# Optimization experiments

Measured on AMD Instinct MI355X. Metric: run time of the kernel, lower is better.

Reference implementation:

```python
import jax, jax.numpy as jnp
import numpy as np

APERTURE = 128
LN_EPS = 1e-6

def _layer_norm(y, g, b):
    mu = jnp.mean(y, axis=-1, keepdims=True)
    var = jnp.var(y, axis=-1, keepdims=True)
    return (y - mu) / jnp.sqrt(var + LN_EPS) * g + b

def setup_inputs() -> dict:
    key = jax.random.key(0)
    ks = jax.random.split(key, 12)
    B, S, D = 4, 4096, 1024
    gain = np.sqrt(2.0)
    xav = lambda k, fan_out, fan_in: jax.random.uniform(
        k, (fan_out, fan_in), jnp.float32,
        -gain * np.sqrt(6.0 / (fan_in + fan_out)), gain * np.sqrt(6.0 / (fan_in + fan_out)))
    return {
        "x": jax.random.normal(ks[0], (B, S, D), jnp.float32),
        "Wq": xav(ks[1], D, D),
        "Wk": xav(ks[2], D, D),
        "Wv": xav(ks[3], D, D),
        "Wo": xav(ks[4], D, D),
        "k1_w": xav(ks[5], D, D),
        "k1_b": jnp.full((D,), 0.1, jnp.float32),
        "k2_w": xav(ks[6], 1, D),
        "k2_b": jnp.full((1,), 0.1, jnp.float32),
        "ln_g": jnp.ones((D,), jnp.float32),
        "ln_b": jnp.zeros((D,), jnp.float32),
    }

def reference(x, Wq, Wk, Wv, Wo, k1_w, k1_b, k2_w, k2_b, ln_g, ln_b):
    B, S, D = x.shape
    scale = jnp.float32(1.0 / np.sqrt(D))
    neg_inf = jnp.float32(-np.inf)

    Q = x @ Wq.T  # [B,S,D]
    K = x @ Wk.T
    V = x @ Wv.T

    e = jnp.einsum('bsd,btd->bst', Q, K) * scale  # [B,S,S]

    # ignore_self: -inf on the diagonal
    i = jnp.arange(S)[:, None]
    j = jnp.arange(S)[None, :]
    e = jnp.where(i == j, neg_inf, e)

    # banded aperture mask: tril(e, ap) * triu(e, -ap); zeros of the product -> -inf
    d = j - i
    scope = jnp.where(d <= APERTURE, e, 0.0) * jnp.where(d >= -APERTURE, e, 0.0)
    e = jnp.where(scope == 0.0, neg_inf, e)

    alpha = jax.nn.softmax(e, axis=2)
    c = jnp.einsum('bst,btd->bsd', alpha, V)
    c = c @ Wo.T

    y = c + x
    y = _layer_norm(y, ln_g, ln_b)
    y = jax.nn.relu(y @ k1_w.T + k1_b)
    y = _layer_norm(y, ln_g, ln_b)
    y = jax.nn.sigmoid(y @ k2_w.T + k2_b)  # [B,S,1]
    return y.reshape(B, S)
```

## Files before the change

kernel.cpp:

```cpp
#include <hip/hip_runtime.h>
#include <math.h>

#define DD 1024
#define SS 4096
#define AP 128
#define LN_EPS 1e-6f
#define BK 32
#define BAND 384

typedef __bf16 bf16;
typedef __attribute__((ext_vector_type(4))) __bf16 bf16x4;
typedef __attribute__((ext_vector_type(8))) __bf16 bf16x8;
typedef __attribute__((ext_vector_type(4))) float f32x4;

#define GLOAD_LDS16(g, l)                                                   \
    __builtin_amdgcn_global_load_lds(                                        \
        (const __attribute__((address_space(1))) void*)(g),                  \
        (__attribute__((address_space(3))) void*)(l), 16, 0, 0)

__global__ __launch_bounds__(256) void prep_all(const float* __restrict__ x,
                                                const float* __restrict__ Wq,
                                                const float* __restrict__ Wk,
                                                const float* __restrict__ Wv,
                                                const float* __restrict__ Wo,
                                                const float* __restrict__ k1w,
                                                const float* __restrict__ k1b,
                                                const float* __restrict__ lng,
                                                const float* __restrict__ lnb,
                                                bf16* __restrict__ xb,
                                                bf16* __restrict__ Wob,
                                                bf16* __restrict__ k1g,
                                                bf16* __restrict__ Wtb,
                                                float* __restrict__ u1,
                                                float* __restrict__ c1b) {
    __shared__ float tile[64][65];
    const int bid = blockIdx.x;
    const int tid = threadIdx.x;
    if (bid < 16384) {
        const int i = (bid * 256 + tid) * 4;
        const float4 a = *(const float4*)(x + i);
        bf16x4 o;
        o[0] = (__bf16)a.x; o[1] = (__bf16)a.y; o[2] = (__bf16)a.z; o[3] = (__bf16)a.w;
        *(bf16x4*)(xb + i) = o;
        return;
    }
    if (bid < 18432) {
        const int b2 = bid - 16384;
        const int sel = b2 >> 10;
        const int bb = b2 & 1023;
        const float* s = sel ? k1w : Wo;
        bf16* d = sel ? k1g : Wob;
        const int i = (bb * 256 + tid) * 4;
        float4 a = *(const float4*)(s + i);
        if (sel) {
            const float4 g4 = *(const float4*)(lng + (i & (DD - 1)));
            a.x *= g4.x; a.y *= g4.y; a.z *= g4.z; a.w *= g4.w;
        }
        bf16x4 o;
        o[0] = (__bf16)a.x; o[1] = (__bf16)a.y; o[2] = (__bf16)a.z; o[3] = (__bf16)a.w;
        *(bf16x4*)(d + i) = o;
        return;
    }
    if (bid < 19200) {
        const int t = bid - 18432;
        const int tz = t >> 8;
        const int tb_ = t & 255;
        const float* in = (tz == 0) ? Wq : (tz == 1) ? Wk : Wv;
        bf16* out = Wtb + ((size_t)tz << 20);
        const int r0 = (tb_ >> 4) * 64, c0 = (tb_ & 15) * 64;
        const int lr = tid >> 4;
        const int lc = (tid & 15) * 4;
#pragma unroll
        for (int rr = 0; rr < 4; rr++) {
            const int row = lr + rr * 16;
            const float4 v = *(const float4*)(in + (size_t)(r0 + row) * DD + c0 + lc);
            tile[row][lc] = v.x; tile[row][lc + 1] = v.y;
            tile[row][lc + 2] = v.z; tile[row][lc + 3] = v.w;
        }
        __syncthreads();
#pragma unroll
        for (int rr = 0; rr < 4; rr++) {
            const int row = lr + rr * 16;
            bf16x4 o;
            o[0] = (__bf16)tile[lc + 0][row];
            o[1] = (__bf16)tile[lc + 1][row];
            o[2] = (__bf16)tile[lc + 2][row];
            o[3] = (__bf16)tile[lc + 3][row];
            *(bf16x4*)(out + (size_t)(c0 + row) * DD + r0 + lc) = o;
        }
        return;
    }
    const int pv = bid - 19200;
    const int lane = tid & 63, wave = tid >> 6;
    const int n = pv * 4 + wave;
    const float* row = k1w + (size_t)n * DD + lane * 16;
    float su = 0.f, sb = 0.f;
#pragma unroll
    for (int q = 0; q < 4; q++) {
        const float4 a = *(const float4*)(row + q * 4);
        const float4 g4 = *(const float4*)(lng + lane * 16 + q * 4);
        const float4 b4 = *(const float4*)(lnb + lane * 16 + q * 4);
        su += a.x * g4.x + a.y * g4.y + a.z * g4.z + a.w * g4.w;
        sb += a.x * b4.x + a.y * b4.y + a.z * b4.z + a.w * b4.w;
    }
#pragma unroll
    for (int off = 32; off > 0; off >>= 1) {
        su += __shfl_xor(su, off);
        sb += __shfl_xor(sb, off);
    }
    if (lane == 0) {
        u1[n] = su;
        c1b[n] = sb + k1b[n];
    }
}

__global__ __launch_bounds__(256) void gemm_pair(const bf16* __restrict__ A0,
                                                 const bf16* __restrict__ W0,
                                                 bf16* __restrict__ O0,
                                                 const bf16* __restrict__ A1,
                                                 const bf16* __restrict__ W1,
                                                 bf16* __restrict__ O1) {
    const bf16* A = blockIdx.z ? A1 : A0;
    const bf16* W = blockIdx.z ? W1 : W0;
    bf16* O = blockIdx.z ? O1 : O0;
    __shared__ bf16 As[128 * BK];
    __shared__ bf16 Bs[128 * BK];
    const int tid = threadIdx.x;
    const int lane = tid & 63;
    const int wave = tid >> 6;
    const int wm = wave & 1;
    const int wn = wave >> 1;
    const int m0 = blockIdx.y * 128;
    const int n0 = blockIdx.x * 128;

    const int c = wave * 64 + lane;
    const int ar = c >> 2;
    const int ac = (c & 3) << 3;
    char* AsB = (char*)As;
    char* BsB = (char*)Bs;
    const int lr = lane & 15;
    const int lk = (lane >> 4) << 3;

    f32x4 acc[4][4] = {};

    for (int kt = 0; kt < DD; kt += BK) {
        const bf16* ga0 = A + (size_t)(m0 + ar) * DD + kt + ac;
        const bf16* gb0 = W + (size_t)(n0 + ar) * DD + kt + ac;
        GLOAD_LDS16(ga0, AsB + wave * 1024);
        GLOAD_LDS16(ga0 + (size_t)64 * DD, AsB + 4096 + wave * 1024);
        GLOAD_LDS16(gb0, BsB + wave * 1024);
        GLOAD_LDS16(gb0 + (size_t)64 * DD, BsB + 4096 + wave * 1024);
        __syncthreads();

        bf16x8 af[4], bfr[4];
#pragma unroll
        for (int i = 0; i < 4; i++)
            af[i] = *(const bf16x8*)&As[(wm * 64 + i * 16 + lr) * BK + lk];
#pragma unroll
        for (int j = 0; j < 4; j++)
            bfr[j] = *(const bf16x8*)&Bs[(wn * 64 + j * 16 + lr) * BK + lk];
#pragma unroll
        for (int i = 0; i < 4; i++)
#pragma unroll
            for (int j = 0; j < 4; j++)
                acc[i][j] = __builtin_amdgcn_mfma_f32_16x16x32_bf16(af[i], bfr[j], acc[i][j], 0, 0, 0);
        __syncthreads();
    }

#pragma unroll
    for (int i = 0; i < 4; i++) {
        const int row = m0 + wm * 64 + i * 16 + ((lane >> 4) << 2);
#pragma unroll
        for (int j = 0; j < 4; j++) {
            const int col = n0 + wn * 64 + j * 16 + (lane & 15);
#pragma unroll
            for (int rr = 0; rr < 4; rr++)
                O[(size_t)(row + rr) * DD + col] = (__bf16)acc[i][j][rr];
        }
    }
}


#define KL_STAGE_A(tt, hh, bb)                                               \
    {                                                                        \
        const bf16* gp_ = Aop + gofsA + (tt) * 64 + (hh) * 32;               \
        GLOAD_LDS16(gp_, smem + (bb) + (hh) * 16384 + ldsW);                 \
        GLOAD_LDS16(gp_ + (size_t)128 * DD,                                  \
                    smem + (bb) + (hh) * 16384 + 8192 + ldsW);               \
    }
#define KL_STAGE_B(tt, hh, bb)                                               \
    {                                                                        \
        const bf16* gp_ = Bop + gofsB + (tt) * 64 + (hh) * 32;               \
        GLOAD_LDS16(gp_, smem + (bb) + 32768 + (hh) * 16384 + ldsW);         \
        GLOAD_LDS16(gp_ + (size_t)128 * DD,                                  \
                    smem + (bb) + 32768 + (hh) * 16384 + 8192 + ldsW);       \
    }
#define KL_READS_A(ks, mh)                                                   \
    af[0] = *(const bf16x8*)(sA + bufo + (ks) * 16384 + (mh) * 4096);        \
    af[1] = *(const bf16x8*)(sA + bufo + (ks) * 16384 + (mh) * 4096 + 1024); \
    af[2] = *(const bf16x8*)(sA + bufo + (ks) * 16384 + (mh) * 4096 + 2048); \
    af[3] = *(const bf16x8*)(sA + bufo + (ks) * 16384 + (mh) * 4096 + 3072);
#define KL_READS_B(ks)                                                       \
    bfr[0] = *(const bf16x8*)(sB + bufo + (ks) * 16384);                     \
    bfr[1] = *(const bf16x8*)(sB + bufo + (ks) * 16384 + 1024);              \
    bfr[2] = *(const bf16x8*)(sB + bufo + (ks) * 16384 + 2048);              \
    bfr[3] = *(const bf16x8*)(sB + bufo + (ks) * 16384 + 3072);
#define KL_MFMA4(I, MH)                                                      \
    acc[(MH) * 4 + I][0] = __builtin_amdgcn_mfma_f32_16x16x32_bf16(af[I], bfr[0], acc[(MH) * 4 + I][0], 0, 0, 0); \
    acc[(MH) * 4 + I][1] = __builtin_amdgcn_mfma_f32_16x16x32_bf16(af[I], bfr[1], acc[(MH) * 4 + I][1], 0, 0, 0); \
    acc[(MH) * 4 + I][2] = __builtin_amdgcn_mfma_f32_16x16x32_bf16(af[I], bfr[2], acc[(MH) * 4 + I][2], 0, 0, 0); \
    acc[(MH) * 4 + I][3] = __builtin_amdgcn_mfma_f32_16x16x32_bf16(af[I], bfr[3], acc[(MH) * 4 + I][3], 0, 0, 0);
#define KL_MFMA16(MH)                                                        \
    __builtin_amdgcn_s_setprio(1);                                           \
    KL_MFMA4(0, MH) KL_MFMA4(1, MH) KL_MFMA4(2, MH) KL_MFMA4(3, MH)          \
    __builtin_amdgcn_s_setprio(0);
#define KL_BARRIER(N) asm volatile("s_waitcnt vmcnt(" #N ")\n\ts_barrier" ::: "memory")

__device__ __forceinline__ void kloop256(const bf16* __restrict__ Aop,
                                         const bf16* __restrict__ Bop,
                                         const int m0, const int n0,
                                         char* smem, f32x4 (&acc)[8][4],
                                         const int tid, const int lane,
                                         const int wave, const int wm, const int wn) {
    const int grow = tid >> 2;
    const int gslot = (tid & 3) ^ ((tid >> 3) & 3);
    const size_t gofsA = (size_t)(m0 + grow) * DD + gslot * 8;
    const size_t gofsB = (size_t)(n0 + grow) * DD + gslot * 8;
    const int ldsW = wave * 1024;
    const int sxo = (((lane >> 4) ^ ((lane >> 1) & 3)) << 4);
    const char* sA = smem + wm * 8192 + (lane & 15) * 64 + sxo;
    const char* sB = smem + 32768 + wn * 4096 + (lane & 15) * 64 + sxo;

    bf16x8 af[4], bfr[4];

    KL_STAGE_A(0, 0, 0) KL_STAGE_B(0, 0, 0)
    KL_STAGE_A(0, 1, 0) KL_STAGE_B(0, 1, 0)
    KL_STAGE_A(1, 0, 65536) KL_STAGE_B(1, 0, 65536)

    int bufo = 0;
    for (int t = 0; t < 15; t++) {
        const int nb = bufo ^ 65536;
        KL_BARRIER(8);
        KL_READS_A(0, 0) KL_READS_B(0)
        KL_STAGE_A(t + 1, 1, nb)
        KL_MFMA16(0)
        KL_READS_A(0, 1)
        KL_STAGE_B(t + 1, 1, nb)
        KL_MFMA16(1)
        KL_BARRIER(8);
        KL_READS_A(1, 0) KL_READS_B(1)
        if (t < 14) { KL_STAGE_A(t + 2, 0, bufo) }
        KL_MFMA16(0)
        KL_READS_A(1, 1)
        if (t < 14) { KL_STAGE_B(t + 2, 0, bufo) }
        KL_MFMA16(1)
        bufo = nb;
    }
    KL_BARRIER(4);
    KL_READS_A(0, 0) KL_READS_B(0)
    KL_MFMA16(0)
    KL_READS_A(0, 1)
    KL_MFMA16(1)
    KL_BARRIER(0);
    KL_READS_A(1, 0) KL_READS_B(1)
    KL_MFMA16(0)
    KL_READS_A(1, 1)
    KL_MFMA16(1)
}

__global__ __launch_bounds__(512) void gemm_uv(const bf16* __restrict__ xb,
                                               const bf16* __restrict__ Gt,
                                               const bf16* __restrict__ W2,
                                               bf16* __restrict__ Ub,
                                               bf16* __restrict__ Vt2) {
    __shared__ char smem[131072];
    int id = blockIdx.x;
    const bf16* A;
    const bf16* W;
    bf16* O;
    int m0, n0;
    size_t ldo;
    if (id < 256) {
        A = xb; W = Gt; O = Ub;
        m0 = (id & 63) * 256; n0 = (id >> 6) * 256; ldo = DD;
    } else {
        id -= 256;
        A = W2; W = xb; O = Vt2;
        m0 = (id >> 6) * 256; n0 = (id & 63) * 256; ldo = (size_t)4 * SS;
    }
    const int tid = threadIdx.x;
    const int lane = tid & 63;
    const int wave = tid >> 6;
    const int wm = wave & 1;
    const int wn = wave >> 1;

    f32x4 acc[8][4] = {};
    kloop256(A, W, m0, n0, smem, acc, tid, lane, wave, wm, wn);

#pragma unroll
    for (int a = 0; a < 8; a++) {
        const int row = m0 + wm * 128 + a * 16 + ((lane >> 4) << 2);
#pragma unroll
        for (int j = 0; j < 4; j++) {
            const int col = n0 + wn * 64 + j * 16 + (lane & 15);
#pragma unroll
            for (int rr = 0; rr < 4; rr++)
                O[(size_t)(row + rr) * ldo + col] = (__bf16)acc[a][j][rr];
        }
    }
}

__global__ __launch_bounds__(512) void gemm_k1(const bf16* __restrict__ T,
                                               const bf16* __restrict__ k1g,
                                               const float* __restrict__ part_t,
                                               const float* __restrict__ u1,
                                               const float* __restrict__ c1b,
                                               const float* __restrict__ lng,
                                               const float* __restrict__ k2w,
                                               float* __restrict__ part_h) {
    __shared__ char smem[131072];
    __shared__ float lmu[256], lrs[256];
    const int m0 = blockIdx.x * 256;
    const int n0 = blockIdx.y * 256;
    const int tid = threadIdx.x;
    const int lane = tid & 63;
    const int wave = tid >> 6;
    const int wm = wave & 1;
    const int wn = wave >> 1;

    if (tid < 256) {
        const float* p = part_t + (size_t)(m0 + tid) * 32;
        float s1 = 0.f, s2 = 0.f;
#pragma unroll
        for (int s = 0; s < 8; s++) {
            const float4 v = *(const float4*)(p + s * 4);
            s1 += v.x + v.z;
            s2 += v.y + v.w;
        }
        const float m = s1 * (1.f / DD);
        lmu[tid] = m;
        lrs[tid] = rsqrtf(s2 * (1.f / DD) - m * m + LN_EPS);
    }
    __syncthreads();

    f32x4 acc[8][4] = {};
    kloop256(T, k1g, m0, n0, smem, acc, tid, lane, wave, wm, wn);

    float u1v[4], cbv[4], ugv[4];
#pragma unroll
    for (int j = 0; j < 4; j++) {
        const int col = n0 + wn * 64 + j * 16 + (lane & 15);
        u1v[j] = u1[col];
        cbv[j] = c1b[col];
        ugv[j] = lng[col] * k2w[col];
    }
    const int strip = blockIdx.y * 4 + wn;
#pragma unroll
    for (int a = 0; a < 8; a++) {
#pragma unroll
        for (int rr = 0; rr < 4; rr++) {
            const int lrow = wm * 128 + a * 16 + ((lane >> 4) << 2) + rr;
            const int row = m0 + lrow;
            const float mr = lmu[lrow], rs = lrs[lrow];
            float s1 = 0.f, s2 = 0.f, s3 = 0.f;
#pragma unroll
            for (int j = 0; j < 4; j++) {
                const float v = rs * (acc[a][j][rr] - mr * u1v[j]) + cbv[j];
                const float h = fmaxf(v, 0.f);
                s1 += h; s2 += h * h; s3 += h * ugv[j];
            }
#pragma unroll
            for (int off = 8; off > 0; off >>= 1) {
                s1 += __shfl_xor(s1, off);
                s2 += __shfl_xor(s2, off);
                s3 += __shfl_xor(s3, off);
            }
            if ((lane & 15) == 0) {
                float* p = part_h + (size_t)row * 48 + strip * 3;
                p[0] = s1; p[1] = s2; p[2] = s3;
            }
        }
    }
}

__global__ __launch_bounds__(256) void attn_s_mfma(const bf16* __restrict__ U,
                                                   const bf16* __restrict__ X,
                                                   float* __restrict__ S) {
    __shared__ bf16 As[128 * BK];
    __shared__ bf16 Bs[128 * BK];
    const int tid = threadIdx.x;
    const int lane = tid & 63;
    const int wave = tid >> 6;
    const int wm = wave & 1;
    const int wn = wave >> 1;
    const int t = blockIdx.x;
    const int nb = blockIdx.y;
    const int m0 = t * 128;
    const long w0 = (long)t * 128 - 128 + (long)nb * 128;

    const int c = wave * 64 + lane;
    const int ar = c >> 2;
    const int ac = (c & 3) << 3;
    char* AsB = (char*)As;
    char* BsB = (char*)Bs;
    const int lr = lane & 15;
    const int lk = (lane >> 4) << 3;

    f32x4 acc[4][4] = {};

    for (int kt = 0; kt < DD; kt += BK) {
        const bf16* ga0 = U + (size_t)(m0 + ar) * DD + kt + ac;
        const bf16* gb0 = X + (w0 + ar) * DD + kt + ac;
        GLOAD_LDS16(ga0, AsB + wave * 1024);
        GLOAD_LDS16(ga0 + (size_t)64 * DD, AsB + 4096 + wave * 1024);
        GLOAD_LDS16(gb0, BsB + wave * 1024);
        GLOAD_LDS16(gb0 + (size_t)64 * DD, BsB + 4096 + wave * 1024);
        __syncthreads();

        bf16x8 af[4], bfr[4];
#pragma unroll
        for (int i = 0; i < 4; i++)
            af[i] = *(const bf16x8*)&As[(wm * 64 + i * 16 + lr) * BK + lk];
#pragma unroll
        for (int j = 0; j < 4; j++)
            bfr[j] = *(const bf16x8*)&Bs[(wn * 64 + j * 16 + lr) * BK + lk];
#pragma unroll
        for (int i = 0; i < 4; i++)
#pragma unroll
            for (int j = 0; j < 4; j++)
                acc[i][j] = __builtin_amdgcn_mfma_f32_16x16x32_bf16(af[i], bfr[j], acc[i][j], 0, 0, 0);
        __syncthreads();
    }

#pragma unroll
    for (int i = 0; i < 4; i++) {
        const int row = m0 + wm * 64 + i * 16 + ((lane >> 4) << 2);
#pragma unroll
        for (int j = 0; j < 4; j++) {
            const int col = nb * 128 + wn * 64 + j * 16 + (lane & 15);
#pragma unroll
            for (int rr = 0; rr < 4; rr++)
                S[(size_t)(row + rr) * BAND + col] = acc[i][j][rr];
        }
    }
}

__global__ __launch_bounds__(256) void attn_softmax(const float* __restrict__ S,
                                                    bf16* __restrict__ P) {
    const int wave = threadIdx.x >> 6;
    const int lane = threadIdx.x & 63;
    const int g = blockIdx.x * 4 + wave;
    const int i = g & (SS - 1);
    const int j_start = ((i >> 7) << 7) - 128;
    const float scale = 0.03125f;
    float s[6];
    float m = -INFINITY;
#pragma unroll
    for (int t = 0; t < 6; t++) {
        const int jj = lane + t * 64;
        const int j = j_start + jj;
        const int dj = j - i;
        const bool valid = (j >= 0) && (j < SS) && (dj != 0) && (dj <= AP) && (dj >= -AP);
        const float v = S[(size_t)g * BAND + jj] * scale;
        s[t] = valid ? v : -INFINITY;
        m = fmaxf(m, s[t]);
    }
#pragma unroll
    for (int off = 32; off > 0; off >>= 1) m = fmaxf(m, __shfl_xor(m, off));
    float l = 0.f;
#pragma unroll
    for (int t = 0; t < 6; t++) {
        s[t] = __expf(s[t] - m);
        l += s[t];
    }
#pragma unroll
    for (int off = 32; off > 0; off >>= 1) l += __shfl_xor(l, off);
    const float inv = 1.f / l;
#pragma unroll
    for (int t = 0; t < 6; t++)
        P[(size_t)g * BAND + lane + t * 64] = (__bf16)(s[t] * inv);
}

__global__ __launch_bounds__(512) void attn_pv_mfma(const bf16* __restrict__ P,
                                                    const bf16* __restrict__ Vt,
                                                    const bf16* __restrict__ xres,
                                                    bf16* __restrict__ T,
                                                    float* __restrict__ part_t) {
    __shared__ bf16 As[128 * BK];
    __shared__ bf16 Bs[256 * BK];
    const int tid = threadIdx.x;
    const int lane = tid & 63;
    const int wave = tid >> 6;
    const int wm = wave & 1;
    const int wn = wave >> 1;
    const int t = blockIdx.x;
    const int m0 = t * 128;
    const int n0 = blockIdx.y * 256;
    const bf16* Wb = Vt + (long)t * 128 - 128;

    const int ar = tid >> 2;
    const int ac = (tid & 3) << 3;
    char* AsB = (char*)As;
    char* BsB = (char*)Bs;
    const int lr = lane & 15;
    const int lk = (lane >> 4) << 3;

    f32x4 acc[4][4] = {};

    for (int kt = 0; kt < BAND; kt += BK) {
        const bf16* ga0 = P + (size_t)(m0 + ar) * BAND + kt + ac;
        const bf16* gb0 = Wb + (size_t)(n0 + ar) * (4 * SS) + kt + ac;
        GLOAD_LDS16(ga0, AsB + wave * 1024);
        GLOAD_LDS16(gb0, BsB + wave * 1024);
        GLOAD_LDS16(gb0 + (size_t)128 * (4 * SS), BsB + 8192 + wave * 1024);
        __syncthreads();

        bf16x8 af[4], bfr[4];
#pragma unroll
        for (int i = 0; i < 4; i++)
            af[i] = *(const bf16x8*)&As[(wm * 64 + i * 16 + lr) * BK + lk];
#pragma unroll
        for (int j = 0; j < 4; j++)
            bfr[j] = *(const bf16x8*)&Bs[(wn * 64 + j * 16 + lr) * BK + lk];
#pragma unroll
        for (int i = 0; i < 4; i++)
#pragma unroll
            for (int j = 0; j < 4; j++)
                acc[i][j] = __builtin_amdgcn_mfma_f32_16x16x32_bf16(af[i], bfr[j], acc[i][j], 0, 0, 0);
        __syncthreads();
    }

    const int strip = blockIdx.y * 4 + wn;
#pragma unroll
    for (int i = 0; i < 4; i++) {
#pragma unroll
        for (int rr = 0; rr < 4; rr++) {
            const int row = m0 + wm * 64 + i * 16 + ((lane >> 4) << 2) + rr;
            float s1 = 0.f, s2 = 0.f;
#pragma unroll
            for (int j = 0; j < 4; j++) {
                const int col = n0 + wn * 64 + j * 16 + (lane & 15);
                const size_t idx = (size_t)row * DD + col;
                const __bf16 tv_b = (__bf16)(acc[i][j][rr] + (float)xres[idx]);
                T[idx] = tv_b;
                const float tv = (float)tv_b;
                s1 += tv; s2 += tv * tv;
            }
#pragma unroll
            for (int off = 8; off > 0; off >>= 1) {
                s1 += __shfl_xor(s1, off);
                s2 += __shfl_xor(s2, off);
            }
            if ((lane & 15) == 0) {
                float2 st; st.x = s1; st.y = s2;
                *(float2*)(part_t + (size_t)row * 32 + strip * 2) = st;
            }
        }
    }
}

__global__ __launch_bounds__(256) void ln_k2_p(const float* __restrict__ part_h,
                                               const float* __restrict__ g,
                                               const float* __restrict__ bta,
                                               const float* __restrict__ w2,
                                               const float* __restrict__ b2,
                                               float* __restrict__ out) {
    __shared__ float red[256], red2[256];
    const int tid = threadIdx.x;
    const float4 g4 = *(const float4*)(g + tid * 4);
    const float4 w4 = *(const float4*)(w2 + tid * 4);
    const float4 b4 = *(const float4*)(bta + tid * 4);
    red[tid] = g4.x * w4.x + g4.y * w4.y + g4.z * w4.z + g4.w * w4.w;
    red2[tid] = b4.x * w4.x + b4.y * w4.y + b4.z * w4.z + b4.w * w4.w;
    __syncthreads();
    for (int s = 128; s > 0; s >>= 1) {
        if (tid < s) { red[tid] += red[tid + s]; red2[tid] += red2[tid + s]; }
        __syncthreads();
    }
    const float sum_u = red[0];
    const float sum_bw = red2[0];

    const int r = blockIdx.x * 256 + tid;
    const float* p = part_h + (size_t)r * 48;
    float s1 = 0.f, s2 = 0.f, s3 = 0.f;
#pragma unroll
    for (int s = 0; s < 16; s++) {
        s1 += p[s * 3 + 0];
        s2 += p[s * 3 + 1];
        s3 += p[s * 3 + 2];
    }
    const float m = s1 * (1.f / DD);
    const float var = s2 * (1.f / DD) - m * m;
    const float rs = rsqrtf(var + LN_EPS);
    const float z = rs * (s3 - m * sum_u) + sum_bw + b2[0];
    out[r] = 1.f / (1.f + __expf(-z));
}

extern "C" void kernel_launch(void* const* d_in, const int* in_sizes, int n_in,
                              void* d_out, int out_size, void* d_ws, size_t ws_size,
                              hipStream_t stream) {
    const float* x   = (const float*)d_in[0];
    const float* Wq  = (const float*)d_in[1];
    const float* Wk  = (const float*)d_in[2];
    const float* Wv  = (const float*)d_in[3];
    const float* Wo  = (const float*)d_in[4];
    const float* k1w = (const float*)d_in[5];
    const float* k1b = (const float*)d_in[6];
    const float* k2w = (const float*)d_in[7];
    const float* k2b = (const float*)d_in[8];
    const float* lng = (const float*)d_in[9];
    const float* lnb = (const float*)d_in[10];
    float* out = (float*)d_out;

    const int N = 4 * SS;
    char* ws = (char*)d_ws;
    bf16*  Ub   = (bf16*)(ws);
    bf16*  xb   = (bf16*)(ws + ((size_t)32  << 20));
    bf16*  Vt2  = (bf16*)(ws + ((size_t)64  << 20));
    bf16*  P    = (bf16*)(ws + ((size_t)96  << 20));
    float* S    = (float*)(ws + ((size_t)108 << 20));
    bf16*  T    = (bf16*)(ws + ((size_t)164 << 20));
    bf16*  Wtb  = (bf16*)(ws + ((size_t)196 << 20));
    bf16*  Wqtb = Wtb;
    bf16*  Wktb = Wqtb + (1 << 20);
    bf16*  Wvtb = Wktb + (1 << 20);
    bf16*  Wob  = Wvtb + (1 << 20);
    bf16*  k1g  = Wob  + (1 << 20);
    bf16*  Gtb  = k1g  + (1 << 20);
    bf16*  W2b  = Gtb  + (1 << 20);
    float* u1     = (float*)(ws + ((size_t)210 << 20));
    float* c1b    = u1 + DD;
    float* part_t = (float*)(ws + ((size_t)211 << 20));
    float* part_h = (float*)(ws + ((size_t)214 << 20));

    dim3 tb(256);

    prep_all<<<19456, tb, 0, stream>>>(x, Wq, Wk, Wv, Wo, k1w, k1b, lng, lnb,
                                       xb, Wob, k1g, Wtb, u1, c1b);

    gemm_pair<<<dim3(8, 8, 2), tb, 0, stream>>>(Wktb, Wqtb, Gtb, Wob, Wvtb, W2b);

    gemm_uv<<<512, dim3(512), 0, stream>>>(xb, Gtb, W2b, Ub, Vt2);

    attn_s_mfma<<<dim3(N / 128, 3), tb, 0, stream>>>(Ub, xb, S);
    attn_softmax<<<N / 4, tb, 0, stream>>>(S, P);
    attn_pv_mfma<<<dim3(N / 128, 4), dim3(512), 0, stream>>>(P, Vt2, xb, T, part_t);

    gemm_k1<<<dim3(64, 4), dim3(512), 0, stream>>>(T, k1g, part_t, u1, c1b, lng, k2w, part_h);
    ln_k2_p<<<N / 256, tb, 0, stream>>>(part_h, lng, lnb, k2w, k2b, out);
}
```

Measured before the change: 334.2 us.

## Double-buffer LDS fragment reads in GEMM k-loop with sched barriers

```diff
diff --git a/kernel.cpp b/kernel.cpp
--- a/kernel.cpp
+++ b/kernel.cpp
@@ -195,26 +195,19 @@
         GLOAD_LDS16(gp_ + (size_t)128 * DD,                                  \
                     smem + (bb) + 32768 + (hh) * 16384 + 8192 + ldsW);       \
     }
-#define KL_READS_A(ks, mh)                                                   \
-    af[0] = *(const bf16x8*)(sA + bufo + (ks) * 16384 + (mh) * 4096);        \
-    af[1] = *(const bf16x8*)(sA + bufo + (ks) * 16384 + (mh) * 4096 + 1024); \
-    af[2] = *(const bf16x8*)(sA + bufo + (ks) * 16384 + (mh) * 4096 + 2048); \
-    af[3] = *(const bf16x8*)(sA + bufo + (ks) * 16384 + (mh) * 4096 + 3072);
-#define KL_READS_B(ks)                                                       \
-    bfr[0] = *(const bf16x8*)(sB + bufo + (ks) * 16384);                     \
-    bfr[1] = *(const bf16x8*)(sB + bufo + (ks) * 16384 + 1024);              \
-    bfr[2] = *(const bf16x8*)(sB + bufo + (ks) * 16384 + 2048);              \
-    bfr[3] = *(const bf16x8*)(sB + bufo + (ks) * 16384 + 3072);
-#define KL_MFMA4(I, MH)                                                      \
-    acc[(MH) * 4 + I][0] = __builtin_amdgcn_mfma_f32_16x16x32_bf16(af[I], bfr[0], acc[(MH) * 4 + I][0], 0, 0, 0); \
-    acc[(MH) * 4 + I][1] = __builtin_amdgcn_mfma_f32_16x16x32_bf16(af[I], bfr[1], acc[(MH) * 4 + I][1], 0, 0, 0); \
-    acc[(MH) * 4 + I][2] = __builtin_amdgcn_mfma_f32_16x16x32_bf16(af[I], bfr[2], acc[(MH) * 4 + I][2], 0, 0, 0); \
-    acc[(MH) * 4 + I][3] = __builtin_amdgcn_mfma_f32_16x16x32_bf16(af[I], bfr[3], acc[(MH) * 4 + I][3], 0, 0, 0);
-#define KL_MFMA16(MH)                                                        \
+#define KL_READS(AR, BR, OFF)                                                \
+    _Pragma("unroll") for (int q_ = 0; q_ < 8; q_++)                         \
+        AR[q_] = *(const bf16x8*)(sA + (OFF) + (q_ >> 2) * 4096 + (q_ & 3) * 1024); \
+    _Pragma("unroll") for (int j_ = 0; j_ < 4; j_++)                         \
+        BR[j_] = *(const bf16x8*)(sB + (OFF) + j_ * 1024);
+#define KL_MFMA32(AR, BR)                                                    \
     __builtin_amdgcn_s_setprio(1);                                           \
-    KL_MFMA4(0, MH) KL_MFMA4(1, MH) KL_MFMA4(2, MH) KL_MFMA4(3, MH)          \
+    _Pragma("unroll") for (int q_ = 0; q_ < 8; q_++)                         \
+        _Pragma("unroll") for (int j_ = 0; j_ < 4; j_++)                     \
+            acc[q_][j_] = __builtin_amdgcn_mfma_f32_16x16x32_bf16(AR[q_], BR[j_], acc[q_][j_], 0, 0, 0); \
     __builtin_amdgcn_s_setprio(0);
 #define KL_BARRIER(N) asm volatile("s_waitcnt vmcnt(" #N ")\n\ts_barrier" ::: "memory")
+#define KL_FENCE __builtin_amdgcn_sched_barrier(0)
 
 __device__ __forceinline__ void kloop256(const bf16* __restrict__ Aop,
                                          const bf16* __restrict__ Bop,
@@ -231,41 +224,45 @@
     const char* sA = smem + wm * 8192 + (lane & 15) * 64 + sxo;
     const char* sB = smem + 32768 + wn * 4096 + (lane & 15) * 64 + sxo;
 
-    bf16x8 af[4], bfr[4];
+    bf16x8 A0[8], B0[4], A1[8], B1[4];
 
     KL_STAGE_A(0, 0, 0) KL_STAGE_B(0, 0, 0)
     KL_STAGE_A(0, 1, 0) KL_STAGE_B(0, 1, 0)
     KL_STAGE_A(1, 0, 65536) KL_STAGE_B(1, 0, 65536)
+    KL_BARRIER(4);
+    KL_READS(A0, B0, 0)
 
     int bufo = 0;
-    for (int t = 0; t < 15; t++) {
+    for (int t = 0; t < 14; t++) {
         const int nb = bufo ^ 65536;
-        KL_BARRIER(8);
-        KL_READS_A(0, 0) KL_READS_B(0)
-        KL_STAGE_A(t + 1, 1, nb)
-        KL_MFMA16(0)
-        KL_READS_A(0, 1)
-        KL_STAGE_B(t + 1, 1, nb)
-        KL_MFMA16(1)
-        KL_BARRIER(8);
-        KL_READS_A(1, 0) KL_READS_B(1)
-        if (t < 14) { KL_STAGE_A(t + 2, 0, bufo) }
-        KL_MFMA16(0)
-        KL_READS_A(1, 1)
-        if (t < 14) { KL_STAGE_B(t + 2, 0, bufo) }
-        KL_MFMA16(1)
+        KL_READS(A1, B1, bufo + 16384)
+        KL_STAGE_A(t + 1, 1, nb) KL_STAGE_B(t + 1, 1, nb)
+        KL_FENCE;
+        KL_MFMA32(A0, B0)
+        KL_BARRIER(4);
+        KL_READS(A0, B0, nb)
+        KL_STAGE_A(t + 2, 0, bufo) KL_STAGE_B(t + 2, 0, bufo)
+        KL_FENCE;
+        KL_MFMA32(A1, B1)
+        KL_BARRIER(4);
         bufo = nb;
     }
-    KL_BARRIER(4);
-    KL_READS_A(0, 0) KL_READS_B(0)
-    KL_MFMA16(0)
-    KL_READS_A(0, 1)
-    KL_MFMA16(1)
-    KL_BARRIER(0);
-    KL_READS_A(1, 0) KL_READS_B(1)
-    KL_MFMA16(0)
-    KL_READS_A(1, 1)
-    KL_MFMA16(1)
+    {
+        const int nb = bufo ^ 65536;
+        KL_READS(A1, B1, bufo + 16384)
+        KL_STAGE_A(15, 1, nb) KL_STAGE_B(15, 1, nb)
+        KL_FENCE;
+        KL_MFMA32(A0, B0)
+        KL_BARRIER(4);
+        KL_READS(A0, B0, nb)
+        KL_FENCE;
+        KL_MFMA32(A1, B1)
+        KL_BARRIER(0);
+        KL_READS(A1, B1, nb + 16384)
+        KL_FENCE;
+        KL_MFMA32(A0, B0)
+        KL_MFMA32(A1, B1)
+    }
 }
 
 __global__ __launch_bounds__(512) void gemm_uv(const bf16* __restrict__ xb,
```

Result: faster. 324.0 us (-3.1%).
